# Kernel optimization log

Hardware: AMD Instinct MI355X
Metric: run time of the kernel (lower is better)

The kernel has to match this reference:

```python
import jax, jax.numpy as jnp
import numpy as np

EPS_COV = 0.01  # module eps added to covariance diagonal
G, N_MEM = 8, 64  # groups, channels per group


def _pade_coeffs(m=5):
    # Taylor coefficients of sqrt(1 - x): c_k = (-1)^k * binom(1/2, k)
    c = np.zeros(2 * m + 1)
    c[0] = 1.0
    b = 1.0
    for k in range(1, 2 * m + 1):
        b *= (0.5 - (k - 1)) / k
        c[k] = ((-1) ** k) * b
    # Pade [m/m]: q_0 = 1, solve sum_j q_j c_{k-j} = 0 for k = m+1..2m
    A = np.zeros((m, m))
    rhs = np.zeros(m)
    for i in range(m):
        k = m + 1 + i
        for j in range(m):
            A[i, j] = c[k - (j + 1)]
        rhs[i] = -c[k]
    q = np.concatenate([[1.0], np.linalg.solve(A, rhs)])
    p = np.array([sum(q[j] * c[k - j] for j in range(min(k, m) + 1)) for k in range(m + 1)])
    return p, q

_PADE_P, _PADE_Q = _pade_coeffs(5)


def matrix_pade_approximant(p, I):
    # evaluates the [5/5] Pade approximant of sqrt at p (normalized SPD matrix)
    pp = jnp.asarray(_PADE_P, dtype=p.dtype)
    pq = jnp.asarray(_PADE_Q, dtype=p.dtype)
    p_app = I - p
    p_sqrt = pp[0] * I
    q_sqrt = pq[0] * I
    p_hat = p_app
    for i in range(5):
        p_sqrt = p_sqrt + pp[i + 1] * p_hat
        q_sqrt = q_sqrt + pq[i + 1] * p_hat
        p_hat = p_hat @ p_app
    return jnp.linalg.solve(q_sqrt, p_sqrt)


def mpa_sqrt(M):
    # batched matrix square root via Pade approximant (MPA_Lya.forward)
    normM = jnp.linalg.norm(M, axis=(1, 2))[:, None, None]
    n = M.shape[1]
    I = jnp.broadcast_to(jnp.eye(n, dtype=M.dtype), M.shape)
    return matrix_pade_approximant(M / normM, I) * jnp.sqrt(normM)


def setup_inputs() -> dict:
    key = jax.random.key(0)
    k1, k2 = jax.random.split(key)
    x = jax.random.normal(k1, (32, 512, 64, 64), dtype=jnp.float32)
    weight = jax.random.uniform(k2, (G, N_MEM, 1), dtype=jnp.float32)
    bias = jnp.zeros((G, N_MEM, 1), dtype=jnp.float32)
    return {"x": x, "weight": weight, "bias": bias}


def reference(x, weight, bias):
    N, C, H, W = x.shape
    n_mem = C // G
    xg = jnp.transpose(x, (1, 0, 2, 3)).reshape(G, n_mem, -1)  # (G, n_mem, N*H*W)
    mu = jnp.mean(xg, axis=2, keepdims=True)
    xg = xg - mu
    I = jnp.eye(n_mem, dtype=x.dtype)[None]
    xxt = jnp.einsum('gim,gjm->gij', xg, xg) / (N * H * W) + I * EPS_COV
    subspace = jnp.linalg.inv(mpa_sqrt(xxt))  # ZCA whitening matrix per group
    xr = jnp.einsum('gij,gjm->gim', subspace, xg)
    xr = xr * weight + bias
    xr = xr.reshape(C, N, H, W)
    return jnp.transpose(xr, (1, 0, 2, 3))
```

## Files before the change

kernel.cpp:

```cpp
#include <hip/hip_runtime.h>

#define NBATCH 32
#define CHAN   512
#define HWSZ   4096
#define NG     8
#define NM     64
#define MTOT   (NBATCH * HWSZ)
#define EPSC   0.01f
#define P68    68

typedef _Float16 f16;
typedef _Float16 f16x8 __attribute__((ext_vector_type(8)));
typedef float    f32x4 __attribute__((ext_vector_type(4)));

#define MFMA16(a, b, c) __builtin_amdgcn_mfma_f32_16x16x32_f16(a, b, c, 0, 0, 0)

__global__ __launch_bounds__(256) void gram_k(const float* __restrict__ x,
                                              float* __restrict__ gpart,
                                              float* __restrict__ spart) {
    __shared__ __align__(16) f16 tile[64 * 128];
    __shared__ float red[2][4096];

    const int bid  = blockIdx.x;
    const int g    = bid >> 6;
    const int n    = (bid >> 1) & 31;
    const int half = bid & 1;
    const float* xb = x + ((size_t)(n * CHAN + g * NM)) * HWSZ + half * 2048;

    const int t = threadIdx.x;
    const int w = t >> 6;
    const int l = t & 63;

    f32x4 acc[4][4];
#pragma unroll
    for (int i = 0; i < 4; ++i)
#pragma unroll
        for (int j = 0; j < 4; ++j) acc[i][j] = (f32x4){0.f, 0.f, 0.f, 0.f};
    float fsum[4] = {0.f, 0.f, 0.f, 0.f};

    for (int tt = 0; tt < 16; ++tt) {
        const float* xt = xb + tt * 128;
#pragma unroll
        for (int i = 0; i < 4; ++i) {
            const int p    = t + 256 * i;
            const int ch   = p >> 4;
            const int off8 = (p & 15) * 8;
            const float4 v0 = *(const float4*)(xt + (size_t)ch * HWSZ + off8);
            const float4 v1 = *(const float4*)(xt + (size_t)ch * HWSZ + off8 + 4);
            fsum[i] += (v0.x + v0.y) + (v0.z + v0.w) + (v1.x + v1.y) + (v1.z + v1.w);
            f16x8 hv;
            hv[0] = (f16)v0.x; hv[1] = (f16)v0.y; hv[2] = (f16)v0.z; hv[3] = (f16)v0.w;
            hv[4] = (f16)v1.x; hv[5] = (f16)v1.y; hv[6] = (f16)v1.z; hv[7] = (f16)v1.w;
            *(f16x8*)&tile[ch * 128 + (off8 ^ ((ch & 7) << 3))] = hv;
        }
        __syncthreads();

        f16x8 frag[4];
#pragma unroll
        for (int rb = 0; rb < 4; ++rb) {
            const int ch = rb * 16 + (l & 15);
            const int k0 = w * 32 + (l >> 4) * 8;
            frag[rb] = *(const f16x8*)&tile[ch * 128 + (k0 ^ ((ch & 7) << 3))];
        }
#pragma unroll
        for (int i = 0; i < 4; ++i)
#pragma unroll
            for (int j = 0; j < 4; ++j)
                acc[i][j] = MFMA16(frag[i], frag[j], acc[i][j]);
        __syncthreads();
    }

#pragma unroll
    for (int i = 0; i < 4; ++i) {
        fsum[i] += __shfl_xor(fsum[i], 1);
        fsum[i] += __shfl_xor(fsum[i], 2);
        fsum[i] += __shfl_xor(fsum[i], 4);
        fsum[i] += __shfl_xor(fsum[i], 8);
    }
    if ((l & 15) == 0) {
        const int chb = t >> 4;
#pragma unroll
        for (int i = 0; i < 4; ++i)
            spart[(size_t)bid * 64 + chb + 16 * i] = fsum[i];
    }

    if (w >= 2) {
#pragma unroll
        for (int i = 0; i < 4; ++i)
#pragma unroll
            for (int j = 0; j < 4; ++j)
#pragma unroll
                for (int r = 0; r < 4; ++r) {
                    const int row = i * 16 + (l >> 4) * 4 + r;
                    const int col = j * 16 + (l & 15);
                    red[w - 2][row * 64 + col] = acc[i][j][r];
                }
    }
    __syncthreads();
    if (w < 2) {
#pragma unroll
        for (int i = 0; i < 4; ++i)
#pragma unroll
            for (int j = 0; j < 4; ++j)
#pragma unroll
                for (int r = 0; r < 4; ++r) {
                    const int row = i * 16 + (l >> 4) * 4 + r;
                    const int col = j * 16 + (l & 15);
                    red[w][row * 64 + col] += acc[i][j][r];
                }
    }
    __syncthreads();
#pragma unroll
    for (int k = 0; k < 16; ++k) {
        const int e = t + 256 * k;
        gpart[(size_t)bid * 4096 + e] = red[0][e] + red[1][e];
    }
}

__global__ __launch_bounds__(256) void solve_k(const float* __restrict__ gpart,
                                               const float* __restrict__ spart,
                                               const float* __restrict__ wgt,
                                               const float* __restrict__ bias,
                                               f16* __restrict__ Tf,
                                               float* __restrict__ offv) {
    __shared__ __align__(16) float A[64 * P68];
    __shared__ __align__(16) float B[64 * P68];
    __shared__ __align__(16) float Cc[64 * P68];
    __shared__ __align__(16) float Dd[64 * P68];
    __shared__ float mus[64];
    __shared__ float red[4];
    __shared__ float tr16[16];

    const int g = blockIdx.x, t = threadIdx.x;

    float covv[16], cov2[16];
#pragma unroll
    for (int k = 0; k < 16; ++k) { covv[k] = 0.f; cov2[k] = 0.f; }
    for (int p = 0; p < 64; p += 2) {
        const float* gp0 = gpart + ((size_t)(g * 64 + p)) * 4096;
        const float* gp1 = gp0 + 4096;
#pragma unroll
        for (int k = 0; k < 16; ++k) {
            covv[k] += gp0[t + 256 * k];
            cov2[k] += gp1[t + 256 * k];
        }
    }
#pragma unroll
    for (int k = 0; k < 16; ++k) covv[k] += cov2[k];

    if (t < 64) {
        float ss = 0.f;
#pragma unroll 8
        for (int p = 0; p < 64; ++p) ss += spart[(size_t)(g * 64 + p) * 64 + t];
        mus[t] = ss * (1.0f / MTOT);
    }
    __syncthreads();

    float loc = 0.f;
#pragma unroll
    for (int k = 0; k < 16; ++k) {
        const int e = t + 256 * k;
        const int i = e >> 6, j = e & 63;
        const float cv = covv[k] * (1.0f / MTOT) - mus[i] * mus[j] + (i == j ? EPSC : 0.f);
        covv[k] = cv;
        loc += cv * cv;
    }
#pragma unroll
    for (int o = 32; o > 0; o >>= 1) loc += __shfl_down(loc, o);
    if ((t & 63) == 0) red[t >> 6] = loc;
    __syncthreads();
    const float normM = sqrtf(red[0] + red[1] + red[2] + red[3]);
    const float ninv  = 1.0f / normM;

#pragma unroll
    for (int k = 0; k < 16; ++k) {
        const int e = t + 256 * k;
        const int i = e >> 6, j = e & 63;
        const float pa = (i == j ? 1.f : 0.f) - covv[k] * ninv;
        A[i * P68 + j] = pa;
        B[i * P68 + j] = pa;
    }
    __syncthreads();

    const int ty = t >> 4, tx = t & 15;
    const int i0 = ty * 4, j0 = tx * 4;

    const float PP[6] = {1.f, -2.75f, 2.75f, -1.203125f, 0.21484375f, -0.0107421875f};
    const float QQ[6] = {1.f, -2.25f, 1.75f, -0.546875f, 0.05859375f, -0.0009765625f};

    float pacc[4][4], qacc[4][4];
#pragma unroll
    for (int ai = 0; ai < 4; ++ai)
#pragma unroll
        for (int bi = 0; bi < 4; ++bi) {
            const int i = i0 + ai, j = j0 + bi;
            const float pa = A[i * P68 + j];
            const float id = (i == j) ? 1.f : 0.f;
            pacc[ai][bi] = PP[0] * id + PP[1] * pa;
            qacc[ai][bi] = QQ[0] * id + QQ[1] * pa;
        }

    float* src = B;
    float* dst = Cc;
    for (int s = 0; s < 4; ++s) {
        float mm[4][4];
#pragma unroll
        for (int ai = 0; ai < 4; ++ai)
#pragma unroll
            for (int bi = 0; bi < 4; ++bi) mm[ai][bi] = 0.f;
        for (int kk = 0; kk < 64; ++kk) {
            const float4 a4 = *(const float4*)&src[kk * P68 + i0];
            const float4 b4 = *(const float4*)&A[kk * P68 + j0];
            const float av[4] = {a4.x, a4.y, a4.z, a4.w};
            const float bv[4] = {b4.x, b4.y, b4.z, b4.w};
#pragma unroll
            for (int ai = 0; ai < 4; ++ai)
#pragma unroll
                for (int bi = 0; bi < 4; ++bi)
                    mm[ai][bi] = fmaf(av[ai], bv[bi], mm[ai][bi]);
        }
#pragma unroll
        for (int ai = 0; ai < 4; ++ai) {
            float4 w4;
            w4.x = mm[ai][0]; w4.y = mm[ai][1]; w4.z = mm[ai][2]; w4.w = mm[ai][3];
            *(float4*)&dst[(i0 + ai) * P68 + j0] = w4;
        }
#pragma unroll
        for (int ai = 0; ai < 4; ++ai)
#pragma unroll
            for (int bi = 0; bi < 4; ++bi) {
                pacc[ai][bi] = fmaf(PP[s + 2], mm[ai][bi], pacc[ai][bi]);
                qacc[ai][bi] = fmaf(QQ[s + 2], mm[ai][bi], qacc[ai][bi]);
            }
        __syncthreads();
        float* tmpp = src; src = dst; dst = tmpp;
    }

    if (ty == tx)
        tr16[tx] = pacc[0][0] + pacc[1][1] + pacc[2][2] + pacc[3][3];
    __syncthreads();
    float trsum = 0.f;
#pragma unroll
    for (int i = 0; i < 16; ++i) trsum += tr16[i];
    const float cP   = trsum * (1.0f / 64.0f);
    const float icP  = 1.0f / cP;

#pragma unroll
    for (int ai = 0; ai < 4; ++ai) {
        float4 we, wq;
        const int i = i0 + ai;
        we.x = pacc[ai][0] * icP - (i == j0 + 0 ? 1.f : 0.f);
        we.y = pacc[ai][1] * icP - (i == j0 + 1 ? 1.f : 0.f);
        we.z = pacc[ai][2] * icP - (i == j0 + 2 ? 1.f : 0.f);
        we.w = pacc[ai][3] * icP - (i == j0 + 3 ? 1.f : 0.f);
        wq.x = qacc[ai][0]; wq.y = qacc[ai][1]; wq.z = qacc[ai][2]; wq.w = qacc[ai][3];
        *(float4*)&A[i * P68 + j0] = we;
        *(float4*)&B[i * P68 + j0] = wq;
    }
    __syncthreads();

    float* rsrc = B;
    float* rdst = Cc;
    for (int it = 0; it < 6; ++it) {
        float mm[4][4];
#pragma unroll
        for (int ai = 0; ai < 4; ++ai)
#pragma unroll
            for (int bi = 0; bi < 4; ++bi) mm[ai][bi] = 0.f;
        for (int kk = 0; kk < 64; ++kk) {
            const float4 a4 = *(const float4*)&A[kk * P68 + i0];
            const float4 b4 = *(const float4*)&rsrc[kk * P68 + j0];
            const float av[4] = {a4.x, a4.y, a4.z, a4.w};
            const float bv[4] = {b4.x, b4.y, b4.z, b4.w};
#pragma unroll
            for (int ai = 0; ai < 4; ++ai)
#pragma unroll
                for (int bi = 0; bi < 4; ++bi)
                    mm[ai][bi] = fmaf(av[ai], bv[bi], mm[ai][bi]);
        }
#pragma unroll
        for (int ai = 0; ai < 4; ++ai) {
            const float4 q4 = *(const float4*)&B[(i0 + ai) * P68 + j0];
            float4 w4;
            w4.x = q4.x - mm[ai][0]; w4.y = q4.y - mm[ai][1];
            w4.z = q4.z - mm[ai][2]; w4.w = q4.w - mm[ai][3];
            *(float4*)&rdst[(i0 + ai) * P68 + j0] = w4;
        }
        __syncthreads();
        if (it == 0) { rsrc = Cc; rdst = Dd; }
        else { float* tmpp = rsrc; rsrc = rdst; rdst = tmpp; }
    }
    float* X = rsrc;

    const float invs = icP / sqrtf(normM);
    if (t < 64) {
        float sm = 0.f;
        for (int j = 0; j < 64; ++j) sm += X[t * P68 + j] * mus[j];
        offv[g * NM + t] = bias[g * NM + t] - sm * invs * wgt[g * NM + t];
    }
#pragma unroll
    for (int k = 0; k < 16; ++k) {
        const int e = t + 256 * k;
        const int i = e >> 6, j = e & 63;
        Tf[(size_t)g * 4096 + e] = (f16)(X[i * P68 + j] * invs * wgt[g * NM + i]);
    }
}

__global__ __launch_bounds__(256) void apply_k(const float* __restrict__ x,
                                               const f16* __restrict__ Tf,
                                               const float* __restrict__ offv,
                                               float* __restrict__ out) {
    __shared__ __align__(16) f16 xs[128 * 64];
    __shared__ __align__(16) f16 Ts[4096];
    __shared__ float offs[64];

    const int bid  = blockIdx.x;
    const int g    = bid >> 6;
    const int n    = (bid >> 1) & 31;
    const int half = bid & 1;
    const size_t base = ((size_t)(n * CHAN + g * NM)) * HWSZ + half * 2048;
    const float* xb = x + base;
    float* ob = out + base;

    const int t = threadIdx.x;
    const int w = t >> 6;
    const int l = t & 63;

#pragma unroll
    for (int i = 0; i < 2; ++i) {
        const int c   = t + 256 * i;
        const int oc  = c >> 3;
        const int icb = (c & 7) * 8;
        const f16x8 v = *(const f16x8*)&Tf[(size_t)g * 4096 + oc * 64 + icb];
        *(f16x8*)&Ts[oc * 64 + (icb ^ ((oc & 7) << 3))] = v;
    }
    if (t < 64) offs[t] = offv[g * NM + t];
    __syncthreads();

    f16x8 afrag[2];
#pragma unroll
    for (int c = 0; c < 2; ++c) {
        const int oc = w * 16 + (l & 15);
        const int k0 = c * 32 + (l >> 4) * 8;
        afrag[c] = *(const f16x8*)&Ts[oc * 64 + (k0 ^ ((oc & 7) << 3))];
    }
    float offr[4];
#pragma unroll
    for (int r = 0; r < 4; ++r) offr[r] = offs[w * 16 + (l >> 4) * 4 + r];

    for (int tt = 0; tt < 16; ++tt) {
        const float* xt = xb + tt * 128;
        __syncthreads();
#pragma unroll
        for (int i = 0; i < 4; ++i) {
            const int p    = t + 256 * i;
            const int ch   = p >> 4;
            const int off8 = (p & 15) * 8;
            const float4 v0 = *(const float4*)(xt + (size_t)ch * HWSZ + off8);
            const float4 v1 = *(const float4*)(xt + (size_t)ch * HWSZ + off8 + 4);
            f16 h[8];
            h[0] = (f16)v0.x; h[1] = (f16)v0.y; h[2] = (f16)v0.z; h[3] = (f16)v0.w;
            h[4] = (f16)v1.x; h[5] = (f16)v1.y; h[6] = (f16)v1.z; h[7] = (f16)v1.w;
#pragma unroll
            for (int j = 0; j < 8; ++j) {
                const int pos = off8 + j;
                xs[pos * 64 + (ch ^ (((pos ^ (pos >> 3)) & 7) << 3))] = h[j];
            }
        }
        __syncthreads();

#pragma unroll
        for (int pb = 0; pb < 8; ++pb) {
            f32x4 acc;
            acc[0] = offr[0]; acc[1] = offr[1]; acc[2] = offr[2]; acc[3] = offr[3];
            const int pos = pb * 16 + (l & 15);
            const int swz = ((pos ^ (pos >> 3)) & 7) << 3;
#pragma unroll
            for (int c = 0; c < 2; ++c) {
                const int k0 = c * 32 + (l >> 4) * 8;
                const f16x8 bfrag = *(const f16x8*)&xs[pos * 64 + (k0 ^ swz)];
                acc = MFMA16(afrag[c], bfrag, acc);
            }
            const int posg = tt * 128 + pb * 16 + (l & 15);
#pragma unroll
            for (int r = 0; r < 4; ++r) {
                const int oc = w * 16 + (l >> 4) * 4 + r;
                ob[(size_t)oc * HWSZ + posg] = acc[r];
            }
        }
    }
}

extern "C" void kernel_launch(void* const* d_in, const int* in_sizes, int n_in,
                              void* d_out, int out_size, void* d_ws, size_t ws_size,
                              hipStream_t stream) {
    const float* x    = (const float*)d_in[0];
    const float* wgt  = (const float*)d_in[1];
    const float* bias = (const float*)d_in[2];
    float* out = (float*)d_out;

    float* ws    = (float*)d_ws;
    float* gpart = ws;
    float* spart = ws + 2097152;
    float* offv  = ws + 2129920;
    f16*   Tf    = (f16*)(ws + 2130432);

    gram_k <<<512, 256, 0, stream>>>(x, gpart, spart);
    solve_k<<<8,   256, 0, stream>>>(gpart, spart, wgt, bias, Tf, offv);
    apply_k<<<512, 256, 0, stream>>>(x, Tf, offv, out);
}
```

Before: 239.8 us.

## Load gram fragments directly, split partial reduction into kernel, double-buffer apply

The gram kernel now loads MFMA fragments straight from global memory into registers, dropping the LDS tile and its barriers. The reduction of 64 partial Gram matrices moves out of the 8-block solve kernel into a separate 128-block reduce kernel, so the reduction runs across more of the GPU. The apply kernel double-buffers the LDS input tile and prefetches the next tile into registers while MFMAs run on the current one. The cost is an extra kernel launch, a workspace round trip, and more registers and LDS in apply.

```diff
diff --git a/kernel.cpp b/kernel.cpp
--- a/kernel.cpp
+++ b/kernel.cpp
@@ -18,8 +18,8 @@
 __global__ __launch_bounds__(256) void gram_k(const float* __restrict__ x,
                                               float* __restrict__ gpart,
                                               float* __restrict__ spart) {
-    __shared__ __align__(16) f16 tile[64 * 128];
     __shared__ float red[2][4096];
+    __shared__ float wsum[4][64];
 
     const int bid  = blockIdx.x;
     const int g    = bid >> 6;
@@ -31,58 +31,49 @@
     const int w = t >> 6;
     const int l = t & 63;
 
+    const float* base = xb + (size_t)(l & 15) * HWSZ + w * 32 + (l >> 4) * 8;
+
     f32x4 acc[4][4];
 #pragma unroll
     for (int i = 0; i < 4; ++i)
 #pragma unroll
         for (int j = 0; j < 4; ++j) acc[i][j] = (f32x4){0.f, 0.f, 0.f, 0.f};
-    float fsum[4] = {0.f, 0.f, 0.f, 0.f};
+    float fs[4] = {0.f, 0.f, 0.f, 0.f};
 
     for (int tt = 0; tt < 16; ++tt) {
-        const float* xt = xb + tt * 128;
-#pragma unroll
-        for (int i = 0; i < 4; ++i) {
-            const int p    = t + 256 * i;
-            const int ch   = p >> 4;
-            const int off8 = (p & 15) * 8;
-            const float4 v0 = *(const float4*)(xt + (size_t)ch * HWSZ + off8);
-            const float4 v1 = *(const float4*)(xt + (size_t)ch * HWSZ + off8 + 4);
-            fsum[i] += (v0.x + v0.y) + (v0.z + v0.w) + (v1.x + v1.y) + (v1.z + v1.w);
+        const float* bt = base + tt * 128;
+        f16x8 frag[4];
+#pragma unroll
+        for (int rb = 0; rb < 4; ++rb) {
+            const float* pr = bt + (size_t)rb * 16 * HWSZ;
+            const float4 v0 = *(const float4*)pr;
+            const float4 v1 = *(const float4*)(pr + 4);
+            fs[rb] += (v0.x + v0.y) + (v0.z + v0.w) + (v1.x + v1.y) + (v1.z + v1.w);
             f16x8 hv;
             hv[0] = (f16)v0.x; hv[1] = (f16)v0.y; hv[2] = (f16)v0.z; hv[3] = (f16)v0.w;
             hv[4] = (f16)v1.x; hv[5] = (f16)v1.y; hv[6] = (f16)v1.z; hv[7] = (f16)v1.w;
-            *(f16x8*)&tile[ch * 128 + (off8 ^ ((ch & 7) << 3))] = hv;
-        }
-        __syncthreads();
-
-        f16x8 frag[4];
-#pragma unroll
-        for (int rb = 0; rb < 4; ++rb) {
-            const int ch = rb * 16 + (l & 15);
-            const int k0 = w * 32 + (l >> 4) * 8;
-            frag[rb] = *(const f16x8*)&tile[ch * 128 + (k0 ^ ((ch & 7) << 3))];
+            frag[rb] = hv;
         }
 #pragma unroll
         for (int i = 0; i < 4; ++i)
 #pragma unroll
             for (int j = 0; j < 4; ++j)
                 acc[i][j] = MFMA16(frag[i], frag[j], acc[i][j]);
-        __syncthreads();
-    }
-
-#pragma unroll
-    for (int i = 0; i < 4; ++i) {
-        fsum[i] += __shfl_xor(fsum[i], 1);
-        fsum[i] += __shfl_xor(fsum[i], 2);
-        fsum[i] += __shfl_xor(fsum[i], 4);
-        fsum[i] += __shfl_xor(fsum[i], 8);
-    }
-    if ((l & 15) == 0) {
-        const int chb = t >> 4;
-#pragma unroll
-        for (int i = 0; i < 4; ++i)
-            spart[(size_t)bid * 64 + chb + 16 * i] = fsum[i];
-    }
+    }
+
+#pragma unroll
+    for (int rb = 0; rb < 4; ++rb) {
+        fs[rb] += __shfl_xor(fs[rb], 16);
+        fs[rb] += __shfl_xor(fs[rb], 32);
+    }
+    if (l < 16) {
+#pragma unroll
+        for (int rb = 0; rb < 4; ++rb) wsum[w][rb * 16 + l] = fs[rb];
+    }
+    __syncthreads();
+    if (t < 64)
+        spart[(size_t)bid * 64 + t] =
+            (wsum[0][t] + wsum[1][t]) + (wsum[2][t] + wsum[3][t]);
 
     if (w >= 2) {
 #pragma unroll
@@ -117,8 +108,25 @@
     }
 }
 
-__global__ __launch_bounds__(256) void solve_k(const float* __restrict__ gpart,
-                                               const float* __restrict__ spart,
+__global__ __launch_bounds__(256) void reduce_k(const float* __restrict__ gpart,
+                                                const float* __restrict__ spart,
+                                                float* __restrict__ gram,
+                                                float* __restrict__ sums) {
+    const int g = blockIdx.x >> 4, c = blockIdx.x & 15;
+    const int t = threadIdx.x;
+    float s = 0.f;
+    for (int p = 0; p < 64; ++p)
+        s += gpart[((size_t)(g * 64 + p)) * 4096 + c * 256 + t];
+    gram[g * 4096 + c * 256 + t] = s;
+    if (c == 0 && t < 64) {
+        float ss = 0.f;
+        for (int p = 0; p < 64; ++p) ss += spart[(size_t)(g * 64 + p) * 64 + t];
+        sums[g * 64 + t] = ss;
+    }
+}
+
+__global__ __launch_bounds__(256) void solve_k(const float* __restrict__ gram,
+                                               const float* __restrict__ sums,
                                                const float* __restrict__ wgt,
                                                const float* __restrict__ bias,
                                                f16* __restrict__ Tf,
@@ -132,36 +140,18 @@
     __shared__ float tr16[16];
 
     const int g = blockIdx.x, t = threadIdx.x;
-
-    float covv[16], cov2[16];
-#pragma unroll
-    for (int k = 0; k < 16; ++k) { covv[k] = 0.f; cov2[k] = 0.f; }
-    for (int p = 0; p < 64; p += 2) {
-        const float* gp0 = gpart + ((size_t)(g * 64 + p)) * 4096;
-        const float* gp1 = gp0 + 4096;
-#pragma unroll
-        for (int k = 0; k < 16; ++k) {
-            covv[k] += gp0[t + 256 * k];
-            cov2[k] += gp1[t + 256 * k];
-        }
-    }
-#pragma unroll
-    for (int k = 0; k < 16; ++k) covv[k] += cov2[k];
-
-    if (t < 64) {
-        float ss = 0.f;
-#pragma unroll 8
-        for (int p = 0; p < 64; ++p) ss += spart[(size_t)(g * 64 + p) * 64 + t];
-        mus[t] = ss * (1.0f / MTOT);
-    }
-    __syncthreads();
-
+    const float* gg = gram + g * 4096;
+
+    if (t < 64) mus[t] = sums[g * NM + t] * (1.0f / MTOT);
+    __syncthreads();
+
+    float covv[16];
     float loc = 0.f;
 #pragma unroll
     for (int k = 0; k < 16; ++k) {
         const int e = t + 256 * k;
         const int i = e >> 6, j = e & 63;
-        const float cv = covv[k] * (1.0f / MTOT) - mus[i] * mus[j] + (i == j ? EPSC : 0.f);
+        const float cv = gg[e] * (1.0f / MTOT) - mus[i] * mus[j] + (i == j ? EPSC : 0.f);
         covv[k] = cv;
         loc += cv * cv;
     }
@@ -242,8 +232,8 @@
     float trsum = 0.f;
 #pragma unroll
     for (int i = 0; i < 16; ++i) trsum += tr16[i];
-    const float cP   = trsum * (1.0f / 64.0f);
-    const float icP  = 1.0f / cP;
+    const float cP  = trsum * (1.0f / 64.0f);
+    const float icP = 1.0f / cP;
 
 #pragma unroll
     for (int ai = 0; ai < 4; ++ai) {
@@ -310,7 +300,7 @@
                                                const f16* __restrict__ Tf,
                                                const float* __restrict__ offv,
                                                float* __restrict__ out) {
-    __shared__ __align__(16) f16 xs[128 * 64];
+    __shared__ __align__(16) f16 xs[2][128 * 64];
     __shared__ __align__(16) f16 Ts[4096];
     __shared__ float offs[64];
 
@@ -335,6 +325,27 @@
         *(f16x8*)&Ts[oc * 64 + (icb ^ ((oc & 7) << 3))] = v;
     }
     if (t < 64) offs[t] = offv[g * NM + t];
+
+    const int chS   = t >> 4;
+    const int off8S = (t & 15) * 8;
+
+    {
+        const float* xt = xb;
+#pragma unroll
+        for (int i = 0; i < 4; ++i) {
+            const int ch = chS + 16 * i;
+            const float4 v0 = *(const float4*)(xt + (size_t)ch * HWSZ + off8S);
+            const float4 v1 = *(const float4*)(xt + (size_t)ch * HWSZ + off8S + 4);
+            f16 h[8];
+            h[0] = (f16)v0.x; h[1] = (f16)v0.y; h[2] = (f16)v0.z; h[3] = (f16)v0.w;
+            h[4] = (f16)v1.x; h[5] = (f16)v1.y; h[6] = (f16)v1.z; h[7] = (f16)v1.w;
+#pragma unroll
+            for (int j = 0; j < 8; ++j) {
+                const int pos = off8S + j;
+                xs[0][pos * 64 + (ch ^ (((pos ^ (pos >> 3)) & 7) << 3))] = h[j];
+            }
+        }
+    }
     __syncthreads();
 
     f16x8 afrag[2];
@@ -349,25 +360,18 @@
     for (int r = 0; r < 4; ++r) offr[r] = offs[w * 16 + (l >> 4) * 4 + r];
 
     for (int tt = 0; tt < 16; ++tt) {
-        const float* xt = xb + tt * 128;
-        __syncthreads();
-#pragma unroll
-        for (int i = 0; i < 4; ++i) {
-            const int p    = t + 256 * i;
-            const int ch   = p >> 4;
-            const int off8 = (p & 15) * 8;
-            const float4 v0 = *(const float4*)(xt + (size_t)ch * HWSZ + off8);
-            const float4 v1 = *(const float4*)(xt + (size_t)ch * HWSZ + off8 + 4);
-            f16 h[8];
-            h[0] = (f16)v0.x; h[1] = (f16)v0.y; h[2] = (f16)v0.z; h[3] = (f16)v0.w;
-            h[4] = (f16)v1.x; h[5] = (f16)v1.y; h[6] = (f16)v1.z; h[7] = (f16)v1.w;
-#pragma unroll
-            for (int j = 0; j < 8; ++j) {
-                const int pos = off8 + j;
-                xs[pos * 64 + (ch ^ (((pos ^ (pos >> 3)) & 7) << 3))] = h[j];
-            }
-        }
-        __syncthreads();
+        const int cur = tt & 1;
+
+        float4 va[4][2];
+        if (tt < 15) {
+            const float* xt = xb + (tt + 1) * 128;
+#pragma unroll
+            for (int i = 0; i < 4; ++i) {
+                const int ch = chS + 16 * i;
+                va[i][0] = *(const float4*)(xt + (size_t)ch * HWSZ + off8S);
+                va[i][1] = *(const float4*)(xt + (size_t)ch * HWSZ + off8S + 4);
+            }
+        }
 
 #pragma unroll
         for (int pb = 0; pb < 8; ++pb) {
@@ -378,7 +382,7 @@
 #pragma unroll
             for (int c = 0; c < 2; ++c) {
                 const int k0 = c * 32 + (l >> 4) * 8;
-                const f16x8 bfrag = *(const f16x8*)&xs[pos * 64 + (k0 ^ swz)];
+                const f16x8 bfrag = *(const f16x8*)&xs[cur][pos * 64 + (k0 ^ swz)];
                 acc = MFMA16(afrag[c], bfrag, acc);
             }
             const int posg = tt * 128 + pb * 16 + (l & 15);
@@ -388,6 +392,24 @@
                 ob[(size_t)oc * HWSZ + posg] = acc[r];
             }
         }
+
+        if (tt < 15) {
+#pragma unroll
+            for (int i = 0; i < 4; ++i) {
+                const int ch = chS + 16 * i;
+                f16 h[8];
+                h[0] = (f16)va[i][0].x; h[1] = (f16)va[i][0].y;
+                h[2] = (f16)va[i][0].z; h[3] = (f16)va[i][0].w;
+                h[4] = (f16)va[i][1].x; h[5] = (f16)va[i][1].y;
+                h[6] = (f16)va[i][1].z; h[7] = (f16)va[i][1].w;
+#pragma unroll
+                for (int j = 0; j < 8; ++j) {
+                    const int pos = off8S + j;
+                    xs[cur ^ 1][pos * 64 + (ch ^ (((pos ^ (pos >> 3)) & 7) << 3))] = h[j];
+                }
+            }
+        }
+        __syncthreads();
     }
 }
 
@@ -402,10 +424,13 @@
     float* ws    = (float*)d_ws;
     float* gpart = ws;
     float* spart = ws + 2097152;
-    float* offv  = ws + 2129920;
-    f16*   Tf    = (f16*)(ws + 2130432);
-
-    gram_k <<<512, 256, 0, stream>>>(x, gpart, spart);
-    solve_k<<<8,   256, 0, stream>>>(gpart, spart, wgt, bias, Tf, offv);
-    apply_k<<<512, 256, 0, stream>>>(x, Tf, offv, out);
+    float* gram  = ws + 2129920;
+    float* sums  = ws + 2162688;
+    float* offv  = ws + 2163200;
+    f16*   Tf    = (f16*)(ws + 2163712);
+
+    gram_k  <<<512, 256, 0, stream>>>(x, gpart, spart);
+    reduce_k<<<128, 256, 0, stream>>>(gpart, spart, gram, sums);
+    solve_k <<<8,   256, 0, stream>>>(gram, sums, wgt, bias, Tf, offv);
+    apply_k <<<512, 256, 0, stream>>>(x, Tf, offv, out);
 }
```

Result: slower. 252.7 us (+5.4%).
